# Kernel tuning notes

Measured on AMD Instinct MI355X. Metric: run time of the kernel, lower is better.

Reference implementation:

```python
import jax, jax.numpy as jnp
import numpy as np

N_NODES = 10000
HEADS = 4
HID = 64
EPS_BN = 1e-5
NEG_SLOPE = 0.2


def gat_conv(x, W, att_src, att_dst, bias, src, dst, heads, out_c, concat):
    """PyG-style GATConv (eval mode, self-loops already appended).
    x: [N, F_in], W: [F_in, heads*out_c], att_*: [heads, out_c], bias: [heads*out_c] or [out_c].
    """
    N = x.shape[0]
    h = (x @ W).reshape(N, heads, out_c)                      # [N,H,C]
    a_s = jnp.sum(h * att_src, axis=-1)                       # [N,H]
    a_d = jnp.sum(h * att_dst, axis=-1)                       # [N,H]
    logits = jax.nn.leaky_relu(a_s[src] + a_d[dst], NEG_SLOPE)  # [E,H]
    # segment softmax over incoming edges of each dst node
    m = jax.ops.segment_max(logits, dst, num_segments=N)
    m = jnp.where(jnp.isfinite(m), m, 0.0)
    e = jnp.exp(logits - m[dst])
    s = jax.ops.segment_sum(e, dst, num_segments=N)
    alpha = e / (s[dst] + 1e-16)                              # [E,H]
    out = jax.ops.segment_sum(h[src] * alpha[..., None], dst, num_segments=N)  # [N,H,C]
    if concat:
        out = out.reshape(N, heads * out_c)
    else:
        out = out.mean(axis=1)
    return out + bias


def batch_norm_eval(x, gamma, beta, mean, var):
    return gamma * (x - mean) * jax.lax.rsqrt(var + EPS_BN) + beta


def setup_inputs() -> dict:
    key = jax.random.key(0)
    ks = jax.random.split(key, 16)
    N, E = N_NODES, 320000
    in_c, hid, H, out_c = 128, HID, HEADS, 64
    x = jax.random.normal(ks[0], (N, in_c), dtype=jnp.float32)
    edge_index = jax.random.randint(ks[1], (2, E), 0, N, dtype=jnp.int32)

    def glorot(k, shape):
        fan = shape[0] + shape[-1]
        return jax.random.normal(k, shape, dtype=jnp.float32) * jnp.sqrt(2.0 / fan)

    return {
        "x": x, "edge_index": edge_index,
        "W0": glorot(ks[2], (in_c, H * hid)),
        "att_src0": glorot(ks[3], (H, hid)), "att_dst0": glorot(ks[4], (H, hid)),
        "b0": jnp.zeros((H * hid,), jnp.float32),
        "g0": jax.random.uniform(ks[5], (H * hid,), jnp.float32, 0.5, 1.5),
        "be0": jax.random.normal(ks[6], (H * hid,), jnp.float32) * 0.1,
        "m0": jnp.zeros((H * hid,), jnp.float32), "v0": jnp.ones((H * hid,), jnp.float32),
        "W1": glorot(ks[7], (H * hid, H * hid)),
        "att_src1": glorot(ks[8], (H, hid)), "att_dst1": glorot(ks[9], (H, hid)),
        "b1": jnp.zeros((H * hid,), jnp.float32),
        "g1": jax.random.uniform(ks[10], (H * hid,), jnp.float32, 0.5, 1.5),
        "be1": jax.random.normal(ks[11], (H * hid,), jnp.float32) * 0.1,
        "m1": jnp.zeros((H * hid,), jnp.float32), "v1": jnp.ones((H * hid,), jnp.float32),
        # layer 2: 256 -> 64, heads=1, concat=False
        "W2": glorot(ks[12], (H * hid, out_c)),
        "att_src2": glorot(ks[13], (1, out_c)), "att_dst2": glorot(ks[14], (1, out_c)),
        "b2": jnp.zeros((out_c,), jnp.float32),
    }


def reference(x, edge_index, W0, att_src0, att_dst0, b0, g0, be0, m0, v0,
              W1, att_src1, att_dst1, b1, g1, be1, m1, v1,
              W2, att_src2, att_dst2, b2):
    N = x.shape[0]
    loops = jnp.arange(N, dtype=edge_index.dtype)
    src = jnp.concatenate([edge_index[0], loops])  # PyG add_self_loops
    dst = jnp.concatenate([edge_index[1], loops])

    h = gat_conv(x, W0, att_src0, att_dst0, b0, src, dst, HEADS, HID, True)
    h = jax.nn.elu(h)
    h = batch_norm_eval(h, g0, be0, m0, v0)

    h = gat_conv(h, W1, att_src1, att_dst1, b1, src, dst, HEADS, HID, True)
    h = jax.nn.elu(h)
    h = batch_norm_eval(h, g1, be1, m1, v1)

    h = gat_conv(h, W2, att_src2, att_dst2, b2, src, dst, 1, 64, False)
    return jax.nn.log_softmax(h, axis=1)
```

## Files before the change

kernel.cpp:

```cpp
#include <hip/hip_runtime.h>
#include <cstdint>
#include <cstddef>

#define NNODES 10000
#define NEDGES 320000
#define NTOT   (NEDGES + NNODES)
#define NPAD   10048
#define NBLK   157

#define BX   5000
#define BW0  128
#define BW1  256
#define BW2  64
#define BH   1250

typedef unsigned short ushort_t;
typedef short bf16x8 __attribute__((ext_vector_type(8)));
typedef float f32x4 __attribute__((ext_vector_type(4)));

__device__ __forceinline__ float lrelu(float x) { return x > 0.f ? x : 0.2f * x; }
__device__ __forceinline__ ushort_t f2b(float v) {
  unsigned b = __float_as_uint(v);
  b += 0x7fffu + ((b >> 16) & 1u);
  return (ushort_t)(b >> 16);
}
__device__ __forceinline__ float blo(unsigned u) { return __uint_as_float(u << 16); }
__device__ __forceinline__ float bhi(unsigned u) { return __uint_as_float(u & 0xffff0000u); }

__global__ __launch_bounds__(256) void prep_kernel(
    const float* __restrict__ x, const float* __restrict__ W0, const float* __restrict__ W1,
    const float* __restrict__ W2, const int* __restrict__ ei,
    ushort_t* __restrict__ xb0, ushort_t* __restrict__ WT0, ushort_t* __restrict__ WT1,
    ushort_t* __restrict__ WT2, int* __restrict__ counts) {
  int b = blockIdx.x;
  int tid = threadIdx.x;
  if (b < BX) { int i = b * 256 + tid; xb0[i] = f2b(x[i]); return; }
  b -= BX;
  if (b < BW0) { int i = b * 256 + tid; int k = i >> 8, m = i & 255; WT0[m * 128 + k] = f2b(W0[i]); return; }
  b -= BW0;
  if (b < BW1) { int i = b * 256 + tid; int k = i >> 8, m = i & 255; WT1[m * 256 + k] = f2b(W1[i]); return; }
  b -= BW1;
  if (b < BW2) { int i = b * 256 + tid; int k = i >> 6, m = i & 63; WT2[m * 256 + k] = f2b(W2[i]); return; }
  b -= BW2;
  { int e = b * 256 + tid; atomicAdd(&counts[ei[NEDGES + e]], 1); }
}

__global__ __launch_bounds__(256) void scan_kernel(
    const int* __restrict__ counts, int* __restrict__ row_ptr,
    int* __restrict__ cursor, int* __restrict__ srcs) {
  __shared__ int lc[NNODES];
  __shared__ int part[256];
  int t = threadIdx.x;
  for (int i = t; i < NNODES; i += 256) lc[i] = counts[i] + 1;
  __syncthreads();
  const int chunk = (NNODES + 255) >> 8;
  int base = t * chunk;
  int s = 0;
  for (int i = 0; i < chunk; ++i) {
    int idx = base + i;
    if (idx < NNODES) s += lc[idx];
  }
  part[t] = s;
  __syncthreads();
  for (int off = 1; off < 256; off <<= 1) {
    int v = (t >= off) ? part[t - off] : 0;
    __syncthreads();
    part[t] += v;
    __syncthreads();
  }
  int run = part[t] - s;
  for (int i = 0; i < chunk; ++i) {
    int idx = base + i;
    if (idx < NNODES) {
      row_ptr[idx] = run;
      srcs[run] = idx;
      cursor[idx] = run + 1;
      run += lc[idx];
    }
  }
  if (t == 255) row_ptr[NNODES] = part[255];
}

template <int K, int H>
__device__ __forceinline__ void gemm_tile(
    const ushort_t* __restrict__ Ab, const ushort_t* __restrict__ WT,
    const float* __restrict__ atts, const float* __restrict__ attd,
    ushort_t* __restrict__ hb, float* __restrict__ a_s, float* __restrict__ a_d,
    int n0, int head) {
  int tid = threadIdx.x, wave = tid >> 6, lane = tid & 63;
  int quad = lane >> 4, l16 = lane & 15;
  int m0 = head * 64;
  const int M = H * 64;
  f32x4 acc[4];
#pragma unroll
  for (int t = 0; t < 4; ++t) acc[t] = (f32x4){0.f, 0.f, 0.f, 0.f};
  const ushort_t* Ap = Ab + (size_t)(n0 + wave * 16 + l16) * K + quad * 8;
  const ushort_t* Wp = WT + (size_t)(m0 + l16) * K + quad * 8;
  for (int k0 = 0; k0 < K; k0 += 32) {
    bf16x8 af = *(const bf16x8*)(Ap + k0);
#pragma unroll
    for (int t = 0; t < 4; ++t) {
      bf16x8 bf = *(const bf16x8*)(Wp + (size_t)t * 16 * K + k0);
      acc[t] = __builtin_amdgcn_mfma_f32_16x16x32_bf16(af, bf, acc[t], 0, 0, 0);
    }
  }
#pragma unroll
  for (int reg = 0; reg < 4; ++reg) {
    int r = n0 + wave * 16 + quad * 4 + reg;
    float ps = 0.f, pd = 0.f;
#pragma unroll
    for (int t = 0; t < 4; ++t) {
      float v = acc[t][reg];
      int col = m0 + t * 16 + l16;
      ps = fmaf(v, atts[col], ps);
      pd = fmaf(v, attd[col], pd);
      if (r < NNODES) hb[(size_t)r * M + col] = f2b(v);
    }
#pragma unroll
    for (int off = 8; off; off >>= 1) {
      ps += __shfl_xor(ps, off);
      pd += __shfl_xor(pd, off);
    }
    if (l16 == 0 && r < NNODES) {
      a_s[r * H + head] = ps;
      a_d[r * H + head] = pd;
    }
  }
}

template <int K, int H>
__global__ __launch_bounds__(256) void gemm_att_kernel(
    const ushort_t* __restrict__ Ab, const ushort_t* __restrict__ WT,
    const float* __restrict__ atts, const float* __restrict__ attd,
    ushort_t* __restrict__ hb, float* __restrict__ a_s, float* __restrict__ a_d) {
  gemm_tile<K, H>(Ab, WT, atts, attd, hb, a_s, a_d, blockIdx.x * 64, blockIdx.y);
}

__global__ __launch_bounds__(256) void gemm0_scatter_kernel(
    const ushort_t* __restrict__ Ab, const ushort_t* __restrict__ WT,
    const float* __restrict__ atts, const float* __restrict__ attd,
    ushort_t* __restrict__ hb, float* __restrict__ a_s, float* __restrict__ a_d,
    const int* __restrict__ ei, int* __restrict__ cursor, int* __restrict__ srcs) {
  int b = blockIdx.x;
  if (b < NBLK * 4) {
    gemm_tile<128, 4>(Ab, WT, atts, attd, hb, a_s, a_d, (b % NBLK) * 64, b / NBLK);
  } else {
    int e = (b - NBLK * 4) * 256 + threadIdx.x;
    if (e < NEDGES) {
      int s = ei[e], d = ei[NEDGES + e];
      srcs[atomicAdd(&cursor[d], 1)] = s;
    }
  }
}

__device__ __forceinline__ void gather8(const char* base, const float* alds, const int* olds,
                                        int cnt, int esub, float acc[8]) {
  int iters = (cnt + 7) >> 3;
  for (int it = 0; it < iters; ++it) {
    int e = it * 8 + esub;
    float a = alds[e];
    int o = olds[e];
    uint4 q = *(const uint4*)(base + o);
    acc[0] = fmaf(a, blo(q.x), acc[0]); acc[1] = fmaf(a, bhi(q.x), acc[1]);
    acc[2] = fmaf(a, blo(q.y), acc[2]); acc[3] = fmaf(a, bhi(q.y), acc[3]);
    acc[4] = fmaf(a, blo(q.z), acc[4]); acc[5] = fmaf(a, bhi(q.z), acc[5]);
    acc[6] = fmaf(a, blo(q.w), acc[6]); acc[7] = fmaf(a, bhi(q.w), acc[7]);
  }
}

__global__ __launch_bounds__(256) void aggregate_kernel(
    const ushort_t* __restrict__ hb16, const float* __restrict__ a_s,
    const float* __restrict__ a_d,
    const int* __restrict__ row_ptr, const int* __restrict__ srcs,
    const float* __restrict__ bias, const float* __restrict__ gam, const float* __restrict__ bet,
    const float* __restrict__ rmean, const float* __restrict__ rvar,
    ushort_t* __restrict__ xb16) {
  __shared__ float s_alpha[4][64];
  __shared__ int s_off[4][64];
  int n = blockIdx.x;
  int hh = threadIdx.x >> 6;
  int lane = threadIdx.x & 63;
  int esub = lane >> 3, csub = lane & 7;
  float* alds = s_alpha[hh];
  int* olds = s_off[hh];
  int jb = row_ptr[n], je = row_ptr[n + 1], deg = je - jb;
  float adn = a_d[n * 4 + hh];
  const char* base = (const char*)hb16 + hh * 128 + csub * 16;
  float acc[8];
#pragma unroll
  for (int i = 0; i < 8; ++i) acc[i] = 0.f;

  if (deg <= 64) {
    int s = (lane < deg) ? srcs[jb + lane] : 0;
    float l = (lane < deg) ? lrelu(a_s[s * 4 + hh] + adn) : -1e30f;
    float mx = l;
#pragma unroll
    for (int off = 32; off; off >>= 1) mx = fmaxf(mx, __shfl_xor(mx, off));
    float e = (lane < deg) ? __expf(l - mx) : 0.f;
    float sum = e;
#pragma unroll
    for (int off = 32; off; off >>= 1) sum += __shfl_xor(sum, off);
    alds[lane] = e / (sum + 1e-16f);
    olds[lane] = s * 512;
    gather8(base, alds, olds, deg, esub, acc);
  } else {
    float mx = -1e30f;
    for (int j = jb + lane; j < je; j += 64)
      mx = fmaxf(mx, lrelu(a_s[srcs[j] * 4 + hh] + adn));
#pragma unroll
    for (int off = 32; off; off >>= 1) mx = fmaxf(mx, __shfl_xor(mx, off));
    float sum = 0.f;
    for (int j = jb + lane; j < je; j += 64)
      sum += __expf(lrelu(a_s[srcs[j] * 4 + hh] + adn) - mx);
#pragma unroll
    for (int off = 32; off; off >>= 1) sum += __shfl_xor(sum, off);
    float inv = 1.0f / (sum + 1e-16f);
    for (int j0 = jb; j0 < je; j0 += 64) {
      int cnt = min(64, je - j0);
      int s = (lane < cnt) ? srcs[j0 + lane] : 0;
      alds[lane] = (lane < cnt) ? __expf(lrelu(a_s[s * 4 + hh] + adn) - mx) * inv : 0.f;
      olds[lane] = s * 512;
      gather8(base, alds, olds, cnt, esub, acc);
    }
  }

#pragma unroll
  for (int i = 0; i < 8; ++i) {
    acc[i] += __shfl_xor(acc[i], 8);
    acc[i] += __shfl_xor(acc[i], 16);
    acc[i] += __shfl_xor(acc[i], 32);
  }
  if (esub == 0) {
    int col0 = hh * 64 + csub * 8;
    float4 bi0 = *(const float4*)&bias[col0],  bi1 = *(const float4*)&bias[col0 + 4];
    float4 gm0 = *(const float4*)&gam[col0],   gm1 = *(const float4*)&gam[col0 + 4];
    float4 bt0 = *(const float4*)&bet[col0],   bt1 = *(const float4*)&bet[col0 + 4];
    float4 rm0 = *(const float4*)&rmean[col0], rm1 = *(const float4*)&rmean[col0 + 4];
    float4 rv0 = *(const float4*)&rvar[col0],  rv1 = *(const float4*)&rvar[col0 + 4];
    float bi[8] = {bi0.x, bi0.y, bi0.z, bi0.w, bi1.x, bi1.y, bi1.z, bi1.w};
    float gm[8] = {gm0.x, gm0.y, gm0.z, gm0.w, gm1.x, gm1.y, gm1.z, gm1.w};
    float bt[8] = {bt0.x, bt0.y, bt0.z, bt0.w, bt1.x, bt1.y, bt1.z, bt1.w};
    float rm[8] = {rm0.x, rm0.y, rm0.z, rm0.w, rm1.x, rm1.y, rm1.z, rm1.w};
    float rv[8] = {rv0.x, rv0.y, rv0.z, rv0.w, rv1.x, rv1.y, rv1.z, rv1.w};
    unsigned pk[4];
#pragma unroll
    for (int i = 0; i < 4; ++i) {
      float v0 = acc[2 * i] + bi[2 * i], v1 = acc[2 * i + 1] + bi[2 * i + 1];
      v0 = v0 > 0.f ? v0 : (__expf(v0) - 1.f);
      v1 = v1 > 0.f ? v1 : (__expf(v1) - 1.f);
      v0 = fmaf(gm[2 * i] * (v0 - rm[2 * i]), rsqrtf(rv[2 * i] + 1e-5f), bt[2 * i]);
      v1 = fmaf(gm[2 * i + 1] * (v1 - rm[2 * i + 1]), rsqrtf(rv[2 * i + 1] + 1e-5f), bt[2 * i + 1]);
      pk[i] = (unsigned)f2b(v0) | ((unsigned)f2b(v1) << 16);
    }
    *(uint4*)((char*)xb16 + (size_t)n * 512 + col0 * 2) = make_uint4(pk[0], pk[1], pk[2], pk[3]);
  }
}

__global__ __launch_bounds__(256) void aggregate2_kernel(
    const ushort_t* __restrict__ hb16, const float* __restrict__ a_s,
    const float* __restrict__ a_d,
    const int* __restrict__ row_ptr, const int* __restrict__ srcs,
    const float* __restrict__ bias, float* __restrict__ out) {
  __shared__ float s_alpha[4][64];
  __shared__ int s_off[4][64];
  int wave = threadIdx.x >> 6;
  int n = blockIdx.x * 4 + wave;
  int lane = threadIdx.x & 63;
  int esub = lane >> 3, csub = lane & 7;
  if (n >= NNODES) return;
  float* alds = s_alpha[wave];
  int* olds = s_off[wave];
  int jb = row_ptr[n], je = row_ptr[n + 1], deg = je - jb;
  float adn = a_d[n];
  const char* base = (const char*)hb16 + csub * 16;
  float acc[8];
#pragma unroll
  for (int i = 0; i < 8; ++i) acc[i] = 0.f;

  if (deg <= 64) {
    int s = (lane < deg) ? srcs[jb + lane] : 0;
    float l = (lane < deg) ? lrelu(a_s[s] + adn) : -1e30f;
    float mx = l;
#pragma unroll
    for (int off = 32; off; off >>= 1) mx = fmaxf(mx, __shfl_xor(mx, off));
    float e = (lane < deg) ? __expf(l - mx) : 0.f;
    float sum = e;
#pragma unroll
    for (int off = 32; off; off >>= 1) sum += __shfl_xor(sum, off);
    alds[lane] = e / (sum + 1e-16f);
    olds[lane] = s * 128;
    gather8(base, alds, olds, deg, esub, acc);
  } else {
    float mx = -1e30f;
    for (int j = jb + lane; j < je; j += 64)
      mx = fmaxf(mx, lrelu(a_s[srcs[j]] + adn));
#pragma unroll
    for (int off = 32; off; off >>= 1) mx = fmaxf(mx, __shfl_xor(mx, off));
    float sum = 0.f;
    for (int j = jb + lane; j < je; j += 64)
      sum += __expf(lrelu(a_s[srcs[j]] + adn) - mx);
#pragma unroll
    for (int off = 32; off; off >>= 1) sum += __shfl_xor(sum, off);
    float inv = 1.0f / (sum + 1e-16f);
    for (int j0 = jb; j0 < je; j0 += 64) {
      int cnt = min(64, je - j0);
      int s = (lane < cnt) ? srcs[j0 + lane] : 0;
      alds[lane] = (lane < cnt) ? __expf(lrelu(a_s[s] + adn) - mx) * inv : 0.f;
      olds[lane] = s * 128;
      gather8(base, alds, olds, cnt, esub, acc);
    }
  }

#pragma unroll
  for (int i = 0; i < 8; ++i) {
    acc[i] += __shfl_xor(acc[i], 8);
    acc[i] += __shfl_xor(acc[i], 16);
    acc[i] += __shfl_xor(acc[i], 32);
  }
  int col0 = csub * 8;
  float4 bi0 = *(const float4*)&bias[col0], bi1 = *(const float4*)&bias[col0 + 4];
  float v[8] = {acc[0] + bi0.x, acc[1] + bi0.y, acc[2] + bi0.z, acc[3] + bi0.w,
                acc[4] + bi1.x, acc[5] + bi1.y, acc[6] + bi1.z, acc[7] + bi1.w};
  float mx = v[0];
#pragma unroll
  for (int i = 1; i < 8; ++i) mx = fmaxf(mx, v[i]);
#pragma unroll
  for (int off = 4; off; off >>= 1) mx = fmaxf(mx, __shfl_xor(mx, off));
  float ex = 0.f;
#pragma unroll
  for (int i = 0; i < 8; ++i) ex += __expf(v[i] - mx);
#pragma unroll
  for (int off = 4; off; off >>= 1) ex += __shfl_xor(ex, off);
  float lse = mx + logf(ex);
  if (esub == 0) {
    float4 o0 = make_float4(v[0] - lse, v[1] - lse, v[2] - lse, v[3] - lse);
    float4 o1 = make_float4(v[4] - lse, v[5] - lse, v[6] - lse, v[7] - lse);
    *(float4*)&out[(size_t)n * 64 + col0] = o0;
    *(float4*)&out[(size_t)n * 64 + col0 + 4] = o1;
  }
}

extern "C" void kernel_launch(void* const* d_in, const int* in_sizes, int n_in,
                              void* d_out, int out_size, void* d_ws, size_t ws_size,
                              hipStream_t stream) {
  const float* x = (const float*)d_in[0];
  const int* ei = (const int*)d_in[1];
  const float* W0 = (const float*)d_in[2];
  const float* as0 = (const float*)d_in[3];
  const float* ad0 = (const float*)d_in[4];
  const float* b0 = (const float*)d_in[5];
  const float* g0p = (const float*)d_in[6];
  const float* be0 = (const float*)d_in[7];
  const float* m0p = (const float*)d_in[8];
  const float* v0p = (const float*)d_in[9];
  const float* W1 = (const float*)d_in[10];
  const float* as1 = (const float*)d_in[11];
  const float* ad1 = (const float*)d_in[12];
  const float* b1 = (const float*)d_in[13];
  const float* g1p = (const float*)d_in[14];
  const float* be1 = (const float*)d_in[15];
  const float* m1p = (const float*)d_in[16];
  const float* v1p = (const float*)d_in[17];
  const float* W2 = (const float*)d_in[18];
  const float* as2 = (const float*)d_in[19];
  const float* ad2 = (const float*)d_in[20];
  const float* b2 = (const float*)d_in[21];
  float* out = (float*)d_out;

  char* w = (char*)d_ws;
  auto alloc = [&](size_t bytes) {
    void* r = (void*)w;
    w += (bytes + 255) & ~(size_t)255;
    return r;
  };
  ushort_t* xb0 = (ushort_t*)alloc((size_t)NPAD * 128 * 2);
  ushort_t* xb16 = (ushort_t*)alloc((size_t)NPAD * 256 * 2);
  ushort_t* hb16 = (ushort_t*)alloc((size_t)NNODES * 256 * 2);
  ushort_t* WT0 = (ushort_t*)alloc((size_t)256 * 128 * 2);
  ushort_t* WT1 = (ushort_t*)alloc((size_t)256 * 256 * 2);
  ushort_t* WT2 = (ushort_t*)alloc((size_t)64 * 256 * 2);
  float* a_s = (float*)alloc((size_t)NNODES * 4 * 4);
  float* a_d = (float*)alloc((size_t)NNODES * 4 * 4);
  int* counts = (int*)alloc((size_t)NNODES * 4);
  int* row_ptr = (int*)alloc((size_t)(NNODES + 1) * 4);
  int* cursor = (int*)alloc((size_t)NNODES * 4);
  int* srcs = (int*)alloc((size_t)NTOT * 4);

  hipMemsetAsync(counts, 0, (size_t)NNODES * 4, stream);
  prep_kernel<<<BX + BW0 + BW1 + BW2 + BH, 256, 0, stream>>>(
      x, W0, W1, W2, ei, xb0, WT0, WT1, WT2, counts);
  scan_kernel<<<1, 256, 0, stream>>>(counts, row_ptr, cursor, srcs);
  gemm0_scatter_kernel<<<NBLK * 4 + BH, 256, 0, stream>>>(
      xb0, WT0, as0, ad0, hb16, a_s, a_d, ei, cursor, srcs);
  aggregate_kernel<<<NNODES, 256, 0, stream>>>(hb16, a_s, a_d, row_ptr, srcs,
                                               b0, g0p, be0, m0p, v0p, xb16);
  gemm_att_kernel<256, 4><<<dim3(NBLK, 4), 256, 0, stream>>>(
      xb16, WT1, as1, ad1, hb16, a_s, a_d);
  aggregate_kernel<<<NNODES, 256, 0, stream>>>(hb16, a_s, a_d, row_ptr, srcs,
                                               b1, g1p, be1, m1p, v1p, xb16);
  gemm_att_kernel<256, 1><<<dim3(NBLK, 1), 256, 0, stream>>>(
      xb16, WT2, as2, ad2, hb16, a_s, a_d);
  aggregate2_kernel<<<(NNODES + 3) / 4, 256, 0, stream>>>(hb16, a_s, a_d,
                                                          row_ptr, srcs, b2, out);
}
```

Measured before the change: 271.6 us.

## Fuse attention aggregation with the next layer's GEMM via shared-memory tile

Replaces the separate aggregate and GEMM kernels for layers 0→1 and 1→2 with one kernel. Each 512-thread block aggregates 16 nodes across all heads, writes the bf16 activations into an LDS tile, then runs the MFMA projection and attention-score dot products straight from that tile. This removes the global round-trip of the intermediate activations and two kernel launches, and ping-pongs between two hidden buffers. In exchange there are only 625 blocks, each wave walks its nodes' heads one after another, and only GH waves take part in the GEMM phase.

```diff
diff --git a/kernel.cpp b/kernel.cpp
--- a/kernel.cpp
+++ b/kernel.cpp
@@ -81,16 +81,15 @@
   if (t == 255) row_ptr[NNODES] = part[255];
 }
 
-template <int K, int H>
-__device__ __forceinline__ void gemm_tile(
+__device__ __forceinline__ void gemm_tile0(
     const ushort_t* __restrict__ Ab, const ushort_t* __restrict__ WT,
     const float* __restrict__ atts, const float* __restrict__ attd,
     ushort_t* __restrict__ hb, float* __restrict__ a_s, float* __restrict__ a_d,
     int n0, int head) {
+  const int K = 128, M = 256;
   int tid = threadIdx.x, wave = tid >> 6, lane = tid & 63;
   int quad = lane >> 4, l16 = lane & 15;
   int m0 = head * 64;
-  const int M = H * 64;
   f32x4 acc[4];
 #pragma unroll
   for (int t = 0; t < 4; ++t) acc[t] = (f32x4){0.f, 0.f, 0.f, 0.f};
@@ -122,18 +121,10 @@
       pd += __shfl_xor(pd, off);
     }
     if (l16 == 0 && r < NNODES) {
-      a_s[r * H + head] = ps;
-      a_d[r * H + head] = pd;
-    }
-  }
-}
-
-template <int K, int H>
-__global__ __launch_bounds__(256) void gemm_att_kernel(
-    const ushort_t* __restrict__ Ab, const ushort_t* __restrict__ WT,
-    const float* __restrict__ atts, const float* __restrict__ attd,
-    ushort_t* __restrict__ hb, float* __restrict__ a_s, float* __restrict__ a_d) {
-  gemm_tile<K, H>(Ab, WT, atts, attd, hb, a_s, a_d, blockIdx.x * 64, blockIdx.y);
+      a_s[r * 4 + head] = ps;
+      a_d[r * 4 + head] = pd;
+    }
+  }
 }
 
 __global__ __launch_bounds__(256) void gemm0_scatter_kernel(
@@ -143,7 +134,7 @@
     const int* __restrict__ ei, int* __restrict__ cursor, int* __restrict__ srcs) {
   int b = blockIdx.x;
   if (b < NBLK * 4) {
-    gemm_tile<128, 4>(Ab, WT, atts, attd, hb, a_s, a_d, (b % NBLK) * 64, b / NBLK);
+    gemm_tile0(Ab, WT, atts, attd, hb, a_s, a_d, (b % NBLK) * 64, b / NBLK);
   } else {
     int e = (b - NBLK * 4) * 256 + threadIdx.x;
     if (e < NEDGES) {
@@ -168,91 +159,179 @@
   }
 }
 
-__global__ __launch_bounds__(256) void aggregate_kernel(
-    const ushort_t* __restrict__ hb16, const float* __restrict__ a_s,
-    const float* __restrict__ a_d,
+template <int GH>
+__global__ __launch_bounds__(512, 4) void agg_gemm_kernel(
+    const ushort_t* __restrict__ hbin,
+    const float* __restrict__ a_s_in, const float* __restrict__ a_d_in,
     const int* __restrict__ row_ptr, const int* __restrict__ srcs,
-    const float* __restrict__ bias, const float* __restrict__ gam, const float* __restrict__ bet,
-    const float* __restrict__ rmean, const float* __restrict__ rvar,
-    ushort_t* __restrict__ xb16) {
-  __shared__ float s_alpha[4][64];
-  __shared__ int s_off[4][64];
-  int n = blockIdx.x;
-  int hh = threadIdx.x >> 6;
-  int lane = threadIdx.x & 63;
+    const float* __restrict__ bias, const float* __restrict__ gam,
+    const float* __restrict__ bet, const float* __restrict__ rmean,
+    const float* __restrict__ rvar,
+    const ushort_t* __restrict__ WT,
+    const float* __restrict__ atts, const float* __restrict__ attd,
+    ushort_t* __restrict__ hbout,
+    float* __restrict__ a_s_out, float* __restrict__ a_d_out) {
+  __shared__ ushort_t tile[16 * 264];
+  __shared__ float s_alpha[8][64];
+  __shared__ int s_off[8][64];
+  int tid = threadIdx.x, wave = tid >> 6, lane = tid & 63;
+  int quad = lane >> 4, l16 = lane & 15;
   int esub = lane >> 3, csub = lane & 7;
-  float* alds = s_alpha[hh];
-  int* olds = s_off[hh];
-  int jb = row_ptr[n], je = row_ptr[n + 1], deg = je - jb;
-  float adn = a_d[n * 4 + hh];
-  const char* base = (const char*)hb16 + hh * 128 + csub * 16;
-  float acc[8];
-#pragma unroll
-  for (int i = 0; i < 8; ++i) acc[i] = 0.f;
-
-  if (deg <= 64) {
-    int s = (lane < deg) ? srcs[jb + lane] : 0;
-    float l = (lane < deg) ? lrelu(a_s[s * 4 + hh] + adn) : -1e30f;
-    float mx = l;
-#pragma unroll
-    for (int off = 32; off; off >>= 1) mx = fmaxf(mx, __shfl_xor(mx, off));
-    float e = (lane < deg) ? __expf(l - mx) : 0.f;
-    float sum = e;
-#pragma unroll
-    for (int off = 32; off; off >>= 1) sum += __shfl_xor(sum, off);
-    alds[lane] = e / (sum + 1e-16f);
-    olds[lane] = s * 512;
-    gather8(base, alds, olds, deg, esub, acc);
-  } else {
-    float mx = -1e30f;
-    for (int j = jb + lane; j < je; j += 64)
-      mx = fmaxf(mx, lrelu(a_s[srcs[j] * 4 + hh] + adn));
-#pragma unroll
-    for (int off = 32; off; off >>= 1) mx = fmaxf(mx, __shfl_xor(mx, off));
-    float sum = 0.f;
-    for (int j = jb + lane; j < je; j += 64)
-      sum += __expf(lrelu(a_s[srcs[j] * 4 + hh] + adn) - mx);
-#pragma unroll
-    for (int off = 32; off; off >>= 1) sum += __shfl_xor(sum, off);
-    float inv = 1.0f / (sum + 1e-16f);
-    for (int j0 = jb; j0 < je; j0 += 64) {
-      int cnt = min(64, je - j0);
-      int s = (lane < cnt) ? srcs[j0 + lane] : 0;
-      alds[lane] = (lane < cnt) ? __expf(lrelu(a_s[s * 4 + hh] + adn) - mx) * inv : 0.f;
+  int n0 = blockIdx.x * 16;
+  float* alds = s_alpha[wave];
+  int* olds = s_off[wave];
+
+  for (int i = 0; i < 2; ++i) {
+    int t = wave * 2 + i;
+    int n = n0 + t;
+    int jb = row_ptr[n], je = row_ptr[n + 1], deg = je - jb;
+    float4 ad4 = *(const float4*)&a_d_in[n * 4];
+
+    if (deg <= 64) {
+      int s = (lane < deg) ? srcs[jb + lane] : 0;
+      float4 as4 = make_float4(0.f, 0.f, 0.f, 0.f);
+      if (lane < deg) as4 = *(const float4*)&a_s_in[s * 4];
       olds[lane] = s * 512;
-      gather8(base, alds, olds, cnt, esub, acc);
-    }
-  }
-
-#pragma unroll
-  for (int i = 0; i < 8; ++i) {
-    acc[i] += __shfl_xor(acc[i], 8);
-    acc[i] += __shfl_xor(acc[i], 16);
-    acc[i] += __shfl_xor(acc[i], 32);
-  }
-  if (esub == 0) {
-    int col0 = hh * 64 + csub * 8;
-    float4 bi0 = *(const float4*)&bias[col0],  bi1 = *(const float4*)&bias[col0 + 4];
-    float4 gm0 = *(const float4*)&gam[col0],   gm1 = *(const float4*)&gam[col0 + 4];
-    float4 bt0 = *(const float4*)&bet[col0],   bt1 = *(const float4*)&bet[col0 + 4];
-    float4 rm0 = *(const float4*)&rmean[col0], rm1 = *(const float4*)&rmean[col0 + 4];
-    float4 rv0 = *(const float4*)&rvar[col0],  rv1 = *(const float4*)&rvar[col0 + 4];
-    float bi[8] = {bi0.x, bi0.y, bi0.z, bi0.w, bi1.x, bi1.y, bi1.z, bi1.w};
-    float gm[8] = {gm0.x, gm0.y, gm0.z, gm0.w, gm1.x, gm1.y, gm1.z, gm1.w};
-    float bt[8] = {bt0.x, bt0.y, bt0.z, bt0.w, bt1.x, bt1.y, bt1.z, bt1.w};
-    float rm[8] = {rm0.x, rm0.y, rm0.z, rm0.w, rm1.x, rm1.y, rm1.z, rm1.w};
-    float rv[8] = {rv0.x, rv0.y, rv0.z, rv0.w, rv1.x, rv1.y, rv1.z, rv1.w};
-    unsigned pk[4];
-#pragma unroll
-    for (int i = 0; i < 4; ++i) {
-      float v0 = acc[2 * i] + bi[2 * i], v1 = acc[2 * i + 1] + bi[2 * i + 1];
-      v0 = v0 > 0.f ? v0 : (__expf(v0) - 1.f);
-      v1 = v1 > 0.f ? v1 : (__expf(v1) - 1.f);
-      v0 = fmaf(gm[2 * i] * (v0 - rm[2 * i]), rsqrtf(rv[2 * i] + 1e-5f), bt[2 * i]);
-      v1 = fmaf(gm[2 * i + 1] * (v1 - rm[2 * i + 1]), rsqrtf(rv[2 * i + 1] + 1e-5f), bt[2 * i + 1]);
-      pk[i] = (unsigned)f2b(v0) | ((unsigned)f2b(v1) << 16);
-    }
-    *(uint4*)((char*)xb16 + (size_t)n * 512 + col0 * 2) = make_uint4(pk[0], pk[1], pk[2], pk[3]);
+#pragma unroll
+      for (int hh = 0; hh < 4; ++hh) {
+        float av = hh == 0 ? as4.x : hh == 1 ? as4.y : hh == 2 ? as4.z : as4.w;
+        float dv = hh == 0 ? ad4.x : hh == 1 ? ad4.y : hh == 2 ? ad4.z : ad4.w;
+        float l = (lane < deg) ? lrelu(av + dv) : -1e30f;
+        float mx = l;
+#pragma unroll
+        for (int off = 32; off; off >>= 1) mx = fmaxf(mx, __shfl_xor(mx, off));
+        float e = (lane < deg) ? __expf(l - mx) : 0.f;
+        float sum = e;
+#pragma unroll
+        for (int off = 32; off; off >>= 1) sum += __shfl_xor(sum, off);
+        alds[lane] = e / (sum + 1e-16f);
+
+        const char* base = (const char*)hbin + hh * 128 + csub * 16;
+        float acc[8];
+#pragma unroll
+        for (int k = 0; k < 8; ++k) acc[k] = 0.f;
+        gather8(base, alds, olds, deg, esub, acc);
+#pragma unroll
+        for (int k = 0; k < 8; ++k) {
+          acc[k] += __shfl_xor(acc[k], 8);
+          acc[k] += __shfl_xor(acc[k], 16);
+          acc[k] += __shfl_xor(acc[k], 32);
+        }
+        if (esub == 0) {
+          int col0 = hh * 64 + csub * 8;
+          float4 bi0 = *(const float4*)&bias[col0],  bi1 = *(const float4*)&bias[col0 + 4];
+          float4 gm0 = *(const float4*)&gam[col0],   gm1 = *(const float4*)&gam[col0 + 4];
+          float4 bt0 = *(const float4*)&bet[col0],   bt1 = *(const float4*)&bet[col0 + 4];
+          float4 rm0 = *(const float4*)&rmean[col0], rm1 = *(const float4*)&rmean[col0 + 4];
+          float4 rv0 = *(const float4*)&rvar[col0],  rv1 = *(const float4*)&rvar[col0 + 4];
+          float bi[8] = {bi0.x, bi0.y, bi0.z, bi0.w, bi1.x, bi1.y, bi1.z, bi1.w};
+          float gm[8] = {gm0.x, gm0.y, gm0.z, gm0.w, gm1.x, gm1.y, gm1.z, gm1.w};
+          float bt[8] = {bt0.x, bt0.y, bt0.z, bt0.w, bt1.x, bt1.y, bt1.z, bt1.w};
+          float rm[8] = {rm0.x, rm0.y, rm0.z, rm0.w, rm1.x, rm1.y, rm1.z, rm1.w};
+          float rv[8] = {rv0.x, rv0.y, rv0.z, rv0.w, rv1.x, rv1.y, rv1.z, rv1.w};
+          unsigned pk[4];
+#pragma unroll
+          for (int k = 0; k < 4; ++k) {
+            float v0 = acc[2 * k] + bi[2 * k], v1 = acc[2 * k + 1] + bi[2 * k + 1];
+            v0 = v0 > 0.f ? v0 : (__expf(v0) - 1.f);
+            v1 = v1 > 0.f ? v1 : (__expf(v1) - 1.f);
+            v0 = fmaf(gm[2 * k] * (v0 - rm[2 * k]), rsqrtf(rv[2 * k] + 1e-5f), bt[2 * k]);
+            v1 = fmaf(gm[2 * k + 1] * (v1 - rm[2 * k + 1]), rsqrtf(rv[2 * k + 1] + 1e-5f), bt[2 * k + 1]);
+            pk[k] = (unsigned)f2b(v0) | ((unsigned)f2b(v1) << 16);
+          }
+          *(uint4*)((char*)tile + t * 528 + col0 * 2) = make_uint4(pk[0], pk[1], pk[2], pk[3]);
+        }
+      }
+    } else {
+      for (int hh = 0; hh < 4; ++hh) {
+        float dv = hh == 0 ? ad4.x : hh == 1 ? ad4.y : hh == 2 ? ad4.z : ad4.w;
+        float mx = -1e30f;
+        for (int j = jb + lane; j < je; j += 64)
+          mx = fmaxf(mx, lrelu(a_s_in[srcs[j] * 4 + hh] + dv));
+#pragma unroll
+        for (int off = 32; off; off >>= 1) mx = fmaxf(mx, __shfl_xor(mx, off));
+        float sum = 0.f;
+        for (int j = jb + lane; j < je; j += 64)
+          sum += __expf(lrelu(a_s_in[srcs[j] * 4 + hh] + dv) - mx);
+#pragma unroll
+        for (int off = 32; off; off >>= 1) sum += __shfl_xor(sum, off);
+        float inv = 1.0f / (sum + 1e-16f);
+        const char* base = (const char*)hbin + hh * 128 + csub * 16;
+        float acc[8];
+#pragma unroll
+        for (int k = 0; k < 8; ++k) acc[k] = 0.f;
+        for (int j0 = jb; j0 < je; j0 += 64) {
+          int cnt = min(64, je - j0);
+          int s = (lane < cnt) ? srcs[j0 + lane] : 0;
+          alds[lane] = (lane < cnt) ? __expf(lrelu(a_s_in[s * 4 + hh] + dv) - mx) * inv : 0.f;
+          olds[lane] = s * 512;
+          gather8(base, alds, olds, cnt, esub, acc);
+        }
+#pragma unroll
+        for (int k = 0; k < 8; ++k) {
+          acc[k] += __shfl_xor(acc[k], 8);
+          acc[k] += __shfl_xor(acc[k], 16);
+          acc[k] += __shfl_xor(acc[k], 32);
+        }
+        if (esub == 0) {
+          int col0 = hh * 64 + csub * 8;
+          unsigned pk[4];
+#pragma unroll
+          for (int k = 0; k < 4; ++k) {
+            int c0 = col0 + 2 * k, c1 = col0 + 2 * k + 1;
+            float v0 = acc[2 * k] + bias[c0], v1 = acc[2 * k + 1] + bias[c1];
+            v0 = v0 > 0.f ? v0 : (__expf(v0) - 1.f);
+            v1 = v1 > 0.f ? v1 : (__expf(v1) - 1.f);
+            v0 = fmaf(gam[c0] * (v0 - rmean[c0]), rsqrtf(rvar[c0] + 1e-5f), bet[c0]);
+            v1 = fmaf(gam[c1] * (v1 - rmean[c1]), rsqrtf(rvar[c1] + 1e-5f), bet[c1]);
+            pk[k] = (unsigned)f2b(v0) | ((unsigned)f2b(v1) << 16);
+          }
+          *(uint4*)((char*)tile + t * 528 + col0 * 2) = make_uint4(pk[0], pk[1], pk[2], pk[3]);
+        }
+      }
+    }
+  }
+
+  __syncthreads();
+
+  if (wave < GH) {
+    const int MOUT = GH * 64;
+    int m0 = wave * 64;
+    f32x4 acc4[4];
+#pragma unroll
+    for (int t = 0; t < 4; ++t) acc4[t] = (f32x4){0.f, 0.f, 0.f, 0.f};
+    const ushort_t* Wp = WT + (size_t)(m0 + l16) * 256 + quad * 8;
+    const ushort_t* Tp = tile + l16 * 264 + quad * 8;
+    for (int k0 = 0; k0 < 256; k0 += 32) {
+      bf16x8 af = *(const bf16x8*)(Tp + k0);
+#pragma unroll
+      for (int t = 0; t < 4; ++t) {
+        bf16x8 bf = *(const bf16x8*)(Wp + (size_t)t * 16 * 256 + k0);
+        acc4[t] = __builtin_amdgcn_mfma_f32_16x16x32_bf16(af, bf, acc4[t], 0, 0, 0);
+      }
+    }
+#pragma unroll
+    for (int reg = 0; reg < 4; ++reg) {
+      int r = n0 + quad * 4 + reg;
+      float ps = 0.f, pd = 0.f;
+#pragma unroll
+      for (int t = 0; t < 4; ++t) {
+        float v = acc4[t][reg];
+        int col = m0 + t * 16 + l16;
+        ps = fmaf(v, atts[col], ps);
+        pd = fmaf(v, attd[col], pd);
+        hbout[(size_t)r * MOUT + col] = f2b(v);
+      }
+#pragma unroll
+      for (int off = 8; off; off >>= 1) {
+        ps += __shfl_xor(ps, off);
+        pd += __shfl_xor(pd, off);
+      }
+      if (l16 == 0) {
+        a_s_out[r * GH + wave] = ps;
+        a_d_out[r * GH + wave] = pd;
+      }
+    }
   }
 }
 
@@ -374,13 +453,15 @@
     return r;
   };
   ushort_t* xb0 = (ushort_t*)alloc((size_t)NPAD * 128 * 2);
-  ushort_t* xb16 = (ushort_t*)alloc((size_t)NPAD * 256 * 2);
-  ushort_t* hb16 = (ushort_t*)alloc((size_t)NNODES * 256 * 2);
+  ushort_t* hbA = (ushort_t*)alloc((size_t)NNODES * 256 * 2);
+  ushort_t* hbB = (ushort_t*)alloc((size_t)NNODES * 256 * 2);
   ushort_t* WT0 = (ushort_t*)alloc((size_t)256 * 128 * 2);
   ushort_t* WT1 = (ushort_t*)alloc((size_t)256 * 256 * 2);
   ushort_t* WT2 = (ushort_t*)alloc((size_t)64 * 256 * 2);
-  float* a_s = (float*)alloc((size_t)NNODES * 4 * 4);
-  float* a_d = (float*)alloc((size_t)NNODES * 4 * 4);
+  float* a_sA = (float*)alloc((size_t)NNODES * 4 * 4);
+  float* a_dA = (float*)alloc((size_t)NNODES * 4 * 4);
+  float* a_sB = (float*)alloc((size_t)NNODES * 4 * 4);
+  float* a_dB = (float*)alloc((size_t)NNODES * 4 * 4);
   int* counts = (int*)alloc((size_t)NNODES * 4);
   int* row_ptr = (int*)alloc((size_t)(NNODES + 1) * 4);
   int* cursor = (int*)alloc((size_t)NNODES * 4);
@@ -391,15 +472,13 @@
       x, W0, W1, W2, ei, xb0, WT0, WT1, WT2, counts);
   scan_kernel<<<1, 256, 0, stream>>>(counts, row_ptr, cursor, srcs);
   gemm0_scatter_kernel<<<NBLK * 4 + BH, 256, 0, stream>>>(
-      xb0, WT0, as0, ad0, hb16, a_s, a_d, ei, cursor, srcs);
-  aggregate_kernel<<<NNODES, 256, 0, stream>>>(hb16, a_s, a_d, row_ptr, srcs,
-                                               b0, g0p, be0, m0p, v0p, xb16);
-  gemm_att_kernel<256, 4><<<dim3(NBLK, 4), 256, 0, stream>>>(
-      xb16, WT1, as1, ad1, hb16, a_s, a_d);
-  aggregate_kernel<<<NNODES, 256, 0, stream>>>(hb16, a_s, a_d, row_ptr, srcs,
-                                               b1, g1p, be1, m1p, v1p, xb16);
-  gemm_att_kernel<256, 1><<<dim3(NBLK, 1), 256, 0, stream>>>(
-      xb16, WT2, as2, ad2, hb16, a_s, a_d);
-  aggregate2_kernel<<<(NNODES + 3) / 4, 256, 0, stream>>>(hb16, a_s, a_d,
+      xb0, WT0, as0, ad0, hbA, a_sA, a_dA, ei, cursor, srcs);
+  agg_gemm_kernel<4><<<NNODES / 16, 512, 0, stream>>>(
+      hbA, a_sA, a_dA, row_ptr, srcs, b0, g0p, be0, m0p, v0p,
+      WT1, as1, ad1, hbB, a_sB, a_dB);
+  agg_gemm_kernel<1><<<NNODES / 16, 512, 0, stream>>>(
+      hbB, a_sB, a_dB, row_ptr, srcs, b1, g1p, be1, m1p, v1p,
+      WT2, as2, ad2, hbA, a_sA, a_dA);
+  aggregate2_kernel<<<(NNODES + 3) / 4, 256, 0, stream>>>(hbA, a_sA, a_dA,
                                                           row_ptr, srcs, b2, out);
 }
```

Result: slower. 286.4 us (+5.4%).
